# Performance work log

Hardware: AMD Instinct MI355X
Metric: run time of the kernel (lower is better)

## Reference

```python
import jax, jax.numpy as jnp
import numpy as np

B, N, H, L = 2, 512, 128, 6
NUM_T = 300.0


def setup_inputs() -> dict:
    key = jax.random.key(0)
    ks = iter(jax.random.split(key, 64))
    nrm = lambda *s: jax.random.normal(next(ks), s, dtype=jnp.float32)
    lin = lambda o, i: nrm(o, i) / np.sqrt(i)
    lin3 = lambda o, i: nrm(L, o, i) / np.sqrt(i)  # stacked per-layer weights
    return dict(
        atom_feat=nrm(B, N, 6),
        coord=nrm(B, N, 3),
        radial=jax.random.uniform(next(ks), (B, N, N, 1), dtype=jnp.float32),
        disp=nrm(B, N, N, 3),
        t=jax.random.uniform(next(ks), (B, 1), dtype=jnp.float32) * NUM_T,
        adj_mat=jnp.ones((B, N, N, 1), dtype=bool),
        mask=jnp.ones((B, N), dtype=bool),
        mask2d=jnp.ones((B, N, N, 1), dtype=bool),
        feat_enc_W=lin(H, 6), feat_enc_b=jnp.zeros(H, jnp.float32),
        freq_bands=jnp.linspace(0.0, 1.0, H // 2, dtype=jnp.float32)[None, :],
        combine_W=lin(H, 2 * H), combine_b=jnp.zeros(H, jnp.float32),
        msg_W1=lin3(H, 2 * H + 1), msg_b1=jnp.zeros((L, H), jnp.float32),
        msg_W2=lin3(H, H), msg_b2=jnp.zeros((L, H), jnp.float32),
        feat_W1=lin3(H, 2 * H), feat_b1=jnp.zeros((L, H), jnp.float32),
        feat_W2=lin3(H, H), feat_b2=jnp.zeros((L, H), jnp.float32),
        coord_W1=lin3(H, H), coord_b1=jnp.zeros((L, H), jnp.float32),
        coord_W2=lin3(1, H) * 0.001,  # xavier gain=0.001
        dec_W1=lin(H, H), dec_b1=jnp.zeros(H, jnp.float32),
        dec_W2=lin(3, H), dec_b2=jnp.zeros(3, jnp.float32),
    )


def _forward(atom_feat, coord, radial, disp, t,
             feat_enc_W, feat_enc_b, freq_bands, combine_W, combine_b,
             msg_W1, msg_b1, msg_W2, msg_b2,
             feat_W1, feat_b1, feat_W2, feat_b2,
             coord_W1, coord_b1, coord_W2,
             dec_W1, dec_b1, dec_W2, dec_b2,
             adj_mat, mask, mask2d):
    silu = jax.nn.silu
    radial = 1.0 / (radial + 0.3)  # use_rinv=True
    fenc = atom_feat @ feat_enc_W.T + feat_enc_b            # [B,N,H]
    ang = (t / NUM_T + freq_bands) * (0.5 * jnp.pi)         # [B,H/2]
    tfeat = jnp.concatenate([jnp.sin(ang), jnp.cos(ang)], -1)[:, None, :]
    tfeat = jnp.broadcast_to(tfeat, fenc.shape)
    feat = jnp.concatenate([fenc, tfeat], -1) @ combine_W.T + combine_b
    dt = feat.dtype
    maskf = mask.astype(dt)[..., None]                      # [B,N,1]
    m2f = mask2d.astype(dt)                                 # [B,N,N,1]
    adjf = adj_mat.astype(dt)
    n = feat.shape[1]
    m2nd = m2f * (1.0 - jnp.eye(n, dtype=dt))[None, :, :, None]  # diag removed
    C = jnp.sum(m2nd[:, 0, :, 0], -1, keepdims=True)[:, :, None]  # [B,1,1]

    def step(f, p):
        Wm1, bm1, Wm2, bm2, Wf1, bf1, Wf2, bf2, Wc1, bc1, Wc2 = p
        # fused broadcast-concat -> linear: split Wm1 over [feat_i | feat_j | radial]
        m = silu((f @ Wm1[:, :H].T)[:, :, None, :]
                 + (f @ Wm1[:, H:2 * H].T)[:, None, :, :]
                 + radial * Wm1[:, 2 * H] + bm1)            # [B,N,N,H]
        m = silu(m @ Wm2.T + bm2)
        # coord update (computed per EGCL, discarded by EGNN forward)
        u = silu(m @ Wc1.T + bc1) @ Wc2.T                   # [B,N,N,1]
        cu = C * jnp.sum(jnp.clip(u * disp, -100.0, 100.0) * m2f * m2nd, axis=2)
        msgf = jnp.sum(m * (m2f * adjf), axis=2)            # [B,N,H]
        nf = silu(jnp.concatenate([f, msgf], -1) @ Wf1.T + bf1) @ Wf2.T + bf2
        return nf * maskf, cu * maskf

    feat, _ = jax.lax.scan(step, feat, (msg_W1, msg_b1, msg_W2, msg_b2,
                                        feat_W1, feat_b1, feat_W2, feat_b2,
                                        coord_W1, coord_b1, coord_W2))
    new_feat = (silu(feat @ dec_W1.T + dec_b1) @ dec_W2.T + dec_b2) * maskf
    return new_feat, coord * maskf


def reference(atom_feat, coord, radial, disp, t, adj_mat, mask, mask2d,
              feat_enc_W, feat_enc_b, freq_bands, combine_W, combine_b,
              msg_W1, msg_b1, msg_W2, msg_b2,
              feat_W1, feat_b1, feat_W2, feat_b2,
              coord_W1, coord_b1, coord_W2,
              dec_W1, dec_b1, dec_W2, dec_b2):
    return _forward(atom_feat, coord, radial, disp, t,
                    feat_enc_W, feat_enc_b, freq_bands, combine_W, combine_b,
                    msg_W1, msg_b1, msg_W2, msg_b2,
                    feat_W1, feat_b1, feat_W2, feat_b2,
                    coord_W1, coord_b1, coord_W2,
                    dec_W1, dec_b1, dec_W2, dec_b2,
                    adj_mat, mask, mask2d)
```

## Files before the change

### kernel.cpp

```cpp
#include <hip/hip_runtime.h>
#include <hip/hip_bf16.h>
#include <math.h>


#define BB 2
#define NN 512
#define HH 128
#define LL 6

typedef short bf16x8 __attribute__((ext_vector_type(8)));
typedef float f32x4  __attribute__((ext_vector_type(4)));

__device__ __forceinline__ float silu_f(float x) {
    return x * __builtin_amdgcn_rcpf(1.0f + __expf(-x));
}
__device__ __forceinline__ short f2bf(float x) {
    union { __hip_bfloat16 b; short s; } u; u.b = __float2bfloat16(x); return u.s;
}
__device__ __forceinline__ float lo_bf(unsigned int w) {
    union { unsigned int u; float f; } v; v.u = w << 16; return v.f;
}
__device__ __forceinline__ float hi_bf(unsigned int w) {
    union { unsigned int u; float f; } v; v.u = w & 0xffff0000u; return v.f;
}
__device__ __forceinline__ unsigned int pk2(float a, float b) {
    return ((unsigned int)(unsigned short)f2bf(a)) |
           (((unsigned int)(unsigned short)f2bf(b)) << 16);
}

__global__ __launch_bounds__(128) void k_pack(
    const float* __restrict__ Wm2,  unsigned short* __restrict__ Wm2b,
    const float* __restrict__ Wf1,  unsigned short* __restrict__ Wf1b,
    const float* __restrict__ Wf2,  unsigned short* __restrict__ Wf2b,
    const float* __restrict__ dW1,  unsigned short* __restrict__ dW1b,
    const float* __restrict__ cmbW, unsigned short* __restrict__ cmbWb,
    const float* __restrict__ Wm1,  unsigned short* __restrict__ Wm1b,
    float* __restrict__ w3f)
{
    const int blk = blockIdx.x;
    const int h   = threadIdx.x;

    if (blk < 864) {
        const int idx4 = blk * 128 + h;
        const float* src; unsigned short* dst; int off;
        if      (idx4 < 24576)  { src = Wm2;  dst = Wm2b;  off = idx4; }
        else if (idx4 < 73728)  { src = Wf1;  dst = Wf1b;  off = idx4 - 24576; }
        else if (idx4 < 98304)  { src = Wf2;  dst = Wf2b;  off = idx4 - 73728; }
        else if (idx4 < 102400) { src = dW1;  dst = dW1b;  off = idx4 - 98304; }
        else                    { src = cmbW; dst = cmbWb; off = idx4 - 102400; }
        const float4 v = ((const float4*)src)[off];
        uint2 o; o.x = pk2(v.x, v.y); o.y = pk2(v.z, v.w);
        ((uint2*)dst)[off] = o;
        return;
    }
    const int lh = blk - 864;
    const float* srow = Wm1 + (size_t)lh * 257;
    unsigned short* drow = Wm1b + (size_t)lh * 256;
    drow[h]       = (unsigned short)f2bf(srow[h]);
    drow[h + 128] = (unsigned short)f2bf(srow[h + 128]);
    if (h == 0) w3f[lh] = srow[256];
}

__global__ __launch_bounds__(256) void k_init(
    const float* __restrict__ atom_feat, const float* __restrict__ t,
    const float* __restrict__ feat_enc_W, const float* __restrict__ feat_enc_b,
    const float* __restrict__ freq_bands,
    const unsigned short* __restrict__ cmbWb, const float* __restrict__ combine_b,
    const unsigned short* __restrict__ Wm1b,  const float* __restrict__ bm1,
    float* __restrict__ feat, float* __restrict__ Ahat,
    unsigned short* __restrict__ Bvb)
{
    const int row0 = blockIdx.x * 16;
    const int b    = row0 >> 9;
    const int tid  = threadIdx.x;
    const int w = tid >> 6, lane = tid & 63, r = lane & 15, g = lane >> 4;
    const int rswz = (r & 7) << 4;

    __shared__ float s_af[96];
    __shared__ float s_few[768];
    __shared__ float s_feb[128];
    __shared__ float s_tf[128];
    __shared__ __align__(16) unsigned short catb[16 * 256];
    __shared__ __align__(16) unsigned short fb[16 * 136];

    if (tid < 96) s_af[tid] = atom_feat[row0 * 6 + tid];
    s_few[tid]       = feat_enc_W[tid];
    s_few[tid + 256] = feat_enc_W[tid + 256];
    s_few[tid + 512] = feat_enc_W[tid + 512];
    if (tid < 128) {
        s_feb[tid] = feat_enc_b[tid];
        const float tv  = t[b] * (1.0f / 300.0f);
        const float ang = (tv + freq_bands[tid & 63]) * 1.5707963267948966f;
        s_tf[tid] = (tid < 64) ? sinf(ang) : cosf(ang);
    }
    __syncthreads();

    {
        const int rw = tid >> 4;
        const int h0 = (tid & 15) * 8;
        float f[8];
        #pragma unroll
        for (int u = 0; u < 8; ++u) {
            const int h = h0 + u;
            float acc = s_feb[h];
            #pragma unroll
            for (int k = 0; k < 6; ++k)
                acc = fmaf(s_af[rw * 6 + k], s_few[h * 6 + k], acc);
            f[u] = acc;
        }
        uint4 o;
        o.x = pk2(f[0], f[1]); o.y = pk2(f[2], f[3]);
        o.z = pk2(f[4], f[5]); o.w = pk2(f[6], f[7]);
        char* base = (char*)&catb[rw * 256];
        const int sz = (rw & 7) << 4;
        *(uint4*)(base + ((h0 * 2) ^ sz)) = o;
        uint4 o2;
        o2.x = pk2(s_tf[h0],     s_tf[h0 + 1]); o2.y = pk2(s_tf[h0 + 2], s_tf[h0 + 3]);
        o2.z = pk2(s_tf[h0 + 4], s_tf[h0 + 5]); o2.w = pk2(s_tf[h0 + 6], s_tf[h0 + 7]);
        *(uint4*)(base + ((256 + h0 * 2) ^ sz)) = o2;
    }
    __syncthreads();

    const int c0 = w * 32 + r, c1 = w * 32 + 16 + r;

    f32x4 d1a = {0,0,0,0}, d1b = {0,0,0,0};
    const char* catp = (const char*)catb;
    #pragma unroll
    for (int s = 0; s < 8; ++s) {
        bf16x8 afr = *(const bf16x8*)(catp + r * 512 + ((s*64 + g*16) ^ rswz));
        d1a = __builtin_amdgcn_mfma_f32_16x16x32_bf16(
                  afr, *(const bf16x8*)(cmbWb + (size_t)c0 * 256 + s*32 + g*8), d1a, 0,0,0);
        d1b = __builtin_amdgcn_mfma_f32_16x16x32_bf16(
                  afr, *(const bf16x8*)(cmbWb + (size_t)c1 * 256 + s*32 + g*8), d1b, 0,0,0);
    }
    {
        const float ba = combine_b[c0], bb = combine_b[c1];
        #pragma unroll
        for (int q = 0; q < 4; ++q) {
            const int rw = g * 4 + q;
            const float va = d1a[q] + ba, vb = d1b[q] + bb;
            feat[(size_t)(row0 + rw) * HH + c0] = va;
            feat[(size_t)(row0 + rw) * HH + c1] = vb;
            fb[rw * 136 + c0] = (unsigned short)f2bf(va);
            fb[rw * 136 + c1] = (unsigned short)f2bf(vb);
        }
    }
    __syncthreads();

    const char* fbp = (const char*)fb;
    f32x4 daa = {0,0,0,0}, dab = {0,0,0,0}, dba = {0,0,0,0}, dbb = {0,0,0,0};
    #pragma unroll
    for (int s = 0; s < 4; ++s) {
        bf16x8 afr = *(const bf16x8*)(fbp + r * 272 + s*64 + g*16);
        daa = __builtin_amdgcn_mfma_f32_16x16x32_bf16(
                  afr, *(const bf16x8*)(Wm1b + (size_t)c0*256 + s*32 + g*8), daa, 0,0,0);
        dab = __builtin_amdgcn_mfma_f32_16x16x32_bf16(
                  afr, *(const bf16x8*)(Wm1b + (size_t)c1*256 + s*32 + g*8), dab, 0,0,0);
        dba = __builtin_amdgcn_mfma_f32_16x16x32_bf16(
                  afr, *(const bf16x8*)(Wm1b + (size_t)c0*256 + 128 + s*32 + g*8), dba, 0,0,0);
        dbb = __builtin_amdgcn_mfma_f32_16x16x32_bf16(
                  afr, *(const bf16x8*)(Wm1b + (size_t)c1*256 + 128 + s*32 + g*8), dbb, 0,0,0);
    }
    {
        const float ba = bm1[c0], bb = bm1[c1];
        #pragma unroll
        for (int q = 0; q < 4; ++q) {
            const int rw = g * 4 + q;
            const size_t i0 = (size_t)(row0 + rw) * HH;
            Ahat[i0 + c0] = daa[q] + ba;
            Ahat[i0 + c1] = dab[q] + bb;
            Bvb[i0 + c0]  = (unsigned short)f2bf(dba[q]);
            Bvb[i0 + c1]  = (unsigned short)f2bf(dbb[q]);
        }
    }
}

__global__ __launch_bounds__(256, 2) void k_msg(
    const float* __restrict__ Ahat,
    const unsigned short* __restrict__ Bvb,
    const float* __restrict__ radial,
    const float* __restrict__ w3l,
    const unsigned short* __restrict__ Wm2b,
    const float* __restrict__ bm2,
    float* __restrict__ feat,
    const unsigned short* __restrict__ Wf1b, const float* __restrict__ bf1,
    const unsigned short* __restrict__ Wf2b, const float* __restrict__ bf2,
    const unsigned short* __restrict__ Wm1n, const float* __restrict__ bm1n,
    float* __restrict__ AhatN,
    unsigned short* __restrict__ BvbN,
    const unsigned short* __restrict__ dW1b, const float* __restrict__ db1,
    const float* __restrict__ dW2, const float* __restrict__ db2,
    const float* __restrict__ coord, float* __restrict__ out,
    int mode)
{
    const int blk  = blockIdx.x;
    const int tid  = threadIdx.x;
    const int w    = tid >> 6, lane = tid & 63, r = lane & 15, g = lane >> 4;
    const int ip   = w >> 1, jh = w & 1;
    const int i    = blk * 2 + ip;
    const int b    = i >> 9;
    const int jbase = jh * (NN / 2);

    float a_r[4][8];
    unsigned int w3p[4][4];
    #pragma unroll
    for (int s = 0; s < 4; ++s) {
        const int kb = s * 32 + g * 8;
        *(float4*)&a_r[s][0] = *(const float4*)(Ahat + (size_t)i * HH + kb);
        *(float4*)&a_r[s][4] = *(const float4*)(Ahat + (size_t)i * HH + kb + 4);
        const float4 x0 = *(const float4*)(w3l + kb);
        const float4 x1 = *(const float4*)(w3l + kb + 4);
        w3p[s][0] = pk2(x0.x, x0.y); w3p[s][1] = pk2(x0.z, x0.w);
        w3p[s][2] = pk2(x1.x, x1.y); w3p[s][3] = pk2(x1.z, x1.w);
    }

    bf16x8 bfrag[8][4];
    #pragma unroll
    for (int n = 0; n < 8; ++n)
        #pragma unroll
        for (int s = 0; s < 4; ++s)
            bfrag[n][s] = *(const bf16x8*)(Wm2b + (size_t)(n * 16 + r) * HH
                                           + s * 32 + g * 8);
    float bm2n[8];
    #pragma unroll
    for (int n = 0; n < 8; ++n) bm2n[n] = bm2[n * 16 + r];

    const unsigned short* BvB = Bvb + (size_t)b * NN * HH;
    const float* rad = radial + (size_t)i * NN;

    float msgacc[8];
    #pragma unroll
    for (int n = 0; n < 8; ++n) msgacc[n] = 0.0f;

    uint4 bv[4];
    #pragma unroll
    for (int s = 0; s < 4; ++s)
        bv[s] = *(const uint4*)(BvB + (size_t)(jbase + r) * HH + s * 32 + g * 8);
    float radv = rad[jbase + r];

    for (int c = 0; c < 16; ++c) {
        const float rinv = __builtin_amdgcn_rcpf(radv + 0.3f);

        bf16x8 afrag[4];
        #pragma unroll
        for (int s = 0; s < 4; ++s) {
            union { uint4 q; unsigned int dw[4]; } u; u.q = bv[s];
            union { bf16x8 v; unsigned int dw[4]; } o;
            #pragma unroll
            for (int d2 = 0; d2 < 4; ++d2) {
                const unsigned int bw = u.dw[d2];
                const unsigned int ww = w3p[s][d2];
                const float m0 = silu_f(fmaf(rinv, lo_bf(ww),
                                             a_r[s][d2 * 2]     + lo_bf(bw)));
                const float m1 = silu_f(fmaf(rinv, hi_bf(ww),
                                             a_r[s][d2 * 2 + 1] + hi_bf(bw)));
                o.dw[d2] = pk2(m0, m1);
            }
            afrag[s] = o.v;
        }

        if (c < 15) {
            const int j = jbase + (c + 1) * 16 + r;
            #pragma unroll
            for (int s = 0; s < 4; ++s)
                bv[s] = *(const uint4*)(BvB + (size_t)j * HH + s * 32 + g * 8);
            radv = rad[j];
        }

        #pragma unroll
        for (int n = 0; n < 8; ++n) {
            f32x4 d = {0.f, 0.f, 0.f, 0.f};
            #pragma unroll
            for (int s = 0; s < 4; ++s)
                d = __builtin_amdgcn_mfma_f32_16x16x32_bf16(
                        afrag[s], bfrag[n][s], d, 0, 0, 0);
            msgacc[n] += (silu_f(d[0] + bm2n[n]) + silu_f(d[1] + bm2n[n]))
                       + (silu_f(d[2] + bm2n[n]) + silu_f(d[3] + bm2n[n]));
        }
    }

    #pragma unroll
    for (int n = 0; n < 8; ++n) {
        float v = msgacc[n];
        v += __shfl_xor(v, 16, 64);
        v += __shfl_xor(v, 32, 64);
        msgacc[n] = v;
    }

    __shared__ float red[2][2][HH];
    __shared__ __align__(16) unsigned short catb[2 * 256];
    __shared__ __align__(16) unsigned short hidb[2 * 128];
    __shared__ __align__(16) unsigned short fb[2 * 128];
    __shared__ float hid2[2][HH];

    if (lane < 16) {
        #pragma unroll
        for (int n = 0; n < 8; ++n) red[ip][jh][n * 16 + lane] = msgacc[n];
    }
    __syncthreads();

    if (tid < 64) {
        const int rw = tid >> 5, q4 = tid & 31;
        const float4 f4 = ((const float4*)(feat + (size_t)(blk * 2 + rw) * HH))[q4];
        uint2 o; o.x = pk2(f4.x, f4.y); o.y = pk2(f4.z, f4.w);
        *(uint2*)&catb[rw * 256 + q4 * 4] = o;
    } else if (tid < 128) {
        const int rw = (tid - 64) >> 5, q4 = (tid - 64) & 31;
        const float4 m0 = ((const float4*)&red[rw][0][0])[q4];
        const float4 m1 = ((const float4*)&red[rw][1][0])[q4];
        uint2 o; o.x = pk2(m0.x + m1.x, m0.y + m1.y);
        o.y = pk2(m0.z + m1.z, m0.w + m1.w);
        *(uint2*)&catb[rw * 256 + 128 + q4 * 4] = o;
    }
    __syncthreads();

    const int c0 = w * 32 + r, c1 = w * 32 + 16 + r;
    const int rr = r & 1;

    f32x4 d1a = {0,0,0,0}, d1b = {0,0,0,0};
    #pragma unroll
    for (int s = 0; s < 8; ++s) {
        bf16x8 afr = *(const bf16x8*)((const char*)catb + rr * 512 + s*64 + g*16);
        d1a = __builtin_amdgcn_mfma_f32_16x16x32_bf16(
                  afr, *(const bf16x8*)(Wf1b + (size_t)c0 * 256 + s*32 + g*8), d1a, 0,0,0);
        d1b = __builtin_amdgcn_mfma_f32_16x16x32_bf16(
                  afr, *(const bf16x8*)(Wf1b + (size_t)c1 * 256 + s*32 + g*8), d1b, 0,0,0);
    }
    if (g == 0) {
        #pragma unroll
        for (int q = 0; q < 2; ++q) {
            hidb[q * 128 + c0] = (unsigned short)f2bf(silu_f(d1a[q] + bf1[c0]));
            hidb[q * 128 + c1] = (unsigned short)f2bf(silu_f(d1b[q] + bf1[c1]));
        }
    }
    __syncthreads();

    f32x4 d2a = {0,0,0,0}, d2b = {0,0,0,0};
    #pragma unroll
    for (int s = 0; s < 4; ++s) {
        bf16x8 afr = *(const bf16x8*)((const char*)hidb + rr * 256 + s*64 + g*16);
        d2a = __builtin_amdgcn_mfma_f32_16x16x32_bf16(
                  afr, *(const bf16x8*)(Wf2b + (size_t)c0 * 128 + s*32 + g*8), d2a, 0,0,0);
        d2b = __builtin_amdgcn_mfma_f32_16x16x32_bf16(
                  afr, *(const bf16x8*)(Wf2b + (size_t)c1 * 128 + s*32 + g*8), d2b, 0,0,0);
    }
    if (g == 0) {
        #pragma unroll
        for (int q = 0; q < 2; ++q) {
            const float va = d2a[q] + bf2[c0], vb = d2b[q] + bf2[c1];
            feat[(size_t)(blk * 2 + q) * HH + c0] = va;
            feat[(size_t)(blk * 2 + q) * HH + c1] = vb;
            fb[q * 128 + c0] = (unsigned short)f2bf(va);
            fb[q * 128 + c1] = (unsigned short)f2bf(vb);
        }
    }
    __syncthreads();

    if (mode == 0) {
        f32x4 daa = {0,0,0,0}, dab = {0,0,0,0}, dba = {0,0,0,0}, dbb = {0,0,0,0};
        #pragma unroll
        for (int s = 0; s < 4; ++s) {
            bf16x8 afr = *(const bf16x8*)((const char*)fb + rr * 256 + s*64 + g*16);
            daa = __builtin_amdgcn_mfma_f32_16x16x32_bf16(
                      afr, *(const bf16x8*)(Wm1n + (size_t)c0*256 + s*32 + g*8), daa, 0,0,0);
            dab = __builtin_amdgcn_mfma_f32_16x16x32_bf16(
                      afr, *(const bf16x8*)(Wm1n + (size_t)c1*256 + s*32 + g*8), dab, 0,0,0);
            dba = __builtin_amdgcn_mfma_f32_16x16x32_bf16(
                      afr, *(const bf16x8*)(Wm1n + (size_t)c0*256 + 128 + s*32 + g*8), dba, 0,0,0);
            dbb = __builtin_amdgcn_mfma_f32_16x16x32_bf16(
                      afr, *(const bf16x8*)(Wm1n + (size_t)c1*256 + 128 + s*32 + g*8), dbb, 0,0,0);
        }
        if (g == 0) {
            #pragma unroll
            for (int q = 0; q < 2; ++q) {
                const size_t i0 = (size_t)(blk * 2 + q) * HH;
                AhatN[i0 + c0] = daa[q] + bm1n[c0];
                AhatN[i0 + c1] = dab[q] + bm1n[c1];
                BvbN[i0 + c0]  = (unsigned short)f2bf(dba[q]);
                BvbN[i0 + c1]  = (unsigned short)f2bf(dbb[q]);
            }
        }
    } else {
        f32x4 dda = {0,0,0,0}, ddb = {0,0,0,0};
        #pragma unroll
        for (int s = 0; s < 4; ++s) {
            bf16x8 afr = *(const bf16x8*)((const char*)fb + rr * 256 + s*64 + g*16);
            dda = __builtin_amdgcn_mfma_f32_16x16x32_bf16(
                      afr, *(const bf16x8*)(dW1b + (size_t)c0 * 128 + s*32 + g*8), dda, 0,0,0);
            ddb = __builtin_amdgcn_mfma_f32_16x16x32_bf16(
                      afr, *(const bf16x8*)(dW1b + (size_t)c1 * 128 + s*32 + g*8), ddb, 0,0,0);
        }
        if (g == 0) {
            #pragma unroll
            for (int q = 0; q < 2; ++q) {
                hid2[q][c0] = silu_f(dda[q] + db1[c0]);
                hid2[q][c1] = silu_f(ddb[q] + db1[c1]);
            }
        }
        __syncthreads();
        if (tid < 6) {
            const int rw = tid / 3, c = tid - rw * 3;
            const float4* wr4 = (const float4*)(dW2 + c * HH);
            const float4* h4  = (const float4*)&hid2[rw][0];
            float a0 = db2[c], a1 = 0.f, a2 = 0.f, a3 = 0.f;
            #pragma unroll 8
            for (int k4 = 0; k4 < 32; ++k4) {
                const float4 hv = h4[k4], wv = wr4[k4];
                a0 = fmaf(hv.x, wv.x, a0); a1 = fmaf(hv.y, wv.y, a1);
                a2 = fmaf(hv.z, wv.z, a2); a3 = fmaf(hv.w, wv.w, a3);
            }
            out[(size_t)(blk * 2 + rw) * 3 + c] = (a0 + a1) + (a2 + a3);
        } else if (tid < 12) {
            const int idx = tid - 6;
            const int rw = idx / 3, c = idx - rw * 3;
            out[(size_t)BB * NN * 3 + (size_t)(blk * 2 + rw) * 3 + c] =
                coord[(size_t)(blk * 2 + rw) * 3 + c];
        }
    }
}

extern "C" void kernel_launch(void* const* d_in, const int* in_sizes, int n_in,
                              void* d_out, int out_size, void* d_ws, size_t ws_size,
                              hipStream_t stream) {
    const float* atom_feat  = (const float*)d_in[0];
    const float* coord      = (const float*)d_in[1];
    const float* radial     = (const float*)d_in[2];
    const float* t          = (const float*)d_in[4];
    const float* feat_enc_W = (const float*)d_in[8];
    const float* feat_enc_b = (const float*)d_in[9];
    const float* freq_bands = (const float*)d_in[10];
    const float* combine_W  = (const float*)d_in[11];
    const float* combine_b  = (const float*)d_in[12];
    const float* msg_W1     = (const float*)d_in[13];
    const float* msg_b1     = (const float*)d_in[14];
    const float* msg_W2     = (const float*)d_in[15];
    const float* msg_b2     = (const float*)d_in[16];
    const float* feat_W1    = (const float*)d_in[17];
    const float* feat_b1    = (const float*)d_in[18];
    const float* feat_W2    = (const float*)d_in[19];
    const float* feat_b2    = (const float*)d_in[20];
    const float* dec_W1     = (const float*)d_in[24];
    const float* dec_b1     = (const float*)d_in[25];
    const float* dec_W2     = (const float*)d_in[26];
    const float* dec_b2     = (const float*)d_in[27];

    float* feat  = (float*)d_ws;
    float* Ahat0 = feat  + (size_t)BB * NN * HH;
    float* Ahat1 = Ahat0 + (size_t)BB * NN * HH;
    float* w3f   = Ahat1 + (size_t)BB * NN * HH;
    unsigned short* Bvb0  = (unsigned short*)(w3f + LL * HH);
    unsigned short* Bvb1  = Bvb0  + (size_t)BB * NN * HH;
    unsigned short* Wm1b  = Bvb1  + (size_t)BB * NN * HH;
    unsigned short* Wm2b  = Wm1b  + (size_t)LL * HH * 256;
    unsigned short* Wf1b  = Wm2b  + (size_t)LL * HH * HH;
    unsigned short* Wf2b  = Wf1b  + (size_t)LL * HH * 256;
    unsigned short* dW1b  = Wf2b  + (size_t)LL * HH * HH;
    unsigned short* cmbWb = dW1b  + (size_t)HH * HH;

    k_pack<<<1632, 128, 0, stream>>>(
        msg_W2, Wm2b, feat_W1, Wf1b, feat_W2, Wf2b,
        dec_W1, dW1b, combine_W, cmbWb, msg_W1, Wm1b, w3f);

    k_init<<<BB * NN / 16, 256, 0, stream>>>(
        atom_feat, t, feat_enc_W, feat_enc_b, freq_bands,
        cmbWb, combine_b, Wm1b, msg_b1, feat, Ahat0, Bvb0);

    float*          AhatP[2] = {Ahat0, Ahat1};
    unsigned short* BvbP[2]  = {Bvb0, Bvb1};

    for (int l = 0; l < LL; ++l) {
        const int cur = l & 1, nxt = cur ^ 1;
        const int last = (l == LL - 1);
        k_msg<<<BB * NN / 2, 256, 0, stream>>>(
            AhatP[cur], BvbP[cur], radial, w3f + l * HH,
            Wm2b + (size_t)l * HH * HH, msg_b2 + l * HH,
            feat,
            Wf1b + (size_t)l * HH * 256, feat_b1 + l * HH,
            Wf2b + (size_t)l * HH * HH,  feat_b2 + l * HH,
            Wm1b + (size_t)(last ? 0 : (l + 1)) * HH * 256,
            msg_b1 + (last ? 0 : (l + 1)) * HH,
            AhatP[nxt], BvbP[nxt],
            dW1b, dec_b1, dec_W2, dec_b2,
            coord, (float*)d_out,
            last ? 1 : 0);
    }
}
```

Before: 469.5 us.

## Split message kernel over K halves with LDS exchange, one row per block

Each block now handles a single node i instead of two, and its four waves split into two j-halves times two K-halves of the hidden dimension. Each wave computes only half of the edge-message activations and swaps them through a double-buffered, swizzled LDS buffer, so every wave holds half the Wm2 output columns and half the register fragments. The aim is to cut register pressure (launch bounds raised to 3 blocks per CU) and double the grid for better occupancy. In exchange it adds a __syncthreads per j-chunk and LDS traffic, and the per-node feature MLP tail now leaves three of the four MFMA rows unused.

```diff
diff --git a/kernel.cpp b/kernel.cpp
--- a/kernel.cpp
+++ b/kernel.cpp
@@ -175,7 +175,7 @@
     }
 }
 
-__global__ __launch_bounds__(256, 2) void k_msg(
+__global__ __launch_bounds__(256, 3) void k_msg(
     const float* __restrict__ Ahat,
     const unsigned short* __restrict__ Bvb,
     const float* __restrict__ radial,
@@ -193,19 +193,20 @@
     const float* __restrict__ coord, float* __restrict__ out,
     int mode)
 {
-    const int blk  = blockIdx.x;
+    const int i    = blockIdx.x;
+    const int b    = i >> 9;
     const int tid  = threadIdx.x;
     const int w    = tid >> 6, lane = tid & 63, r = lane & 15, g = lane >> 4;
-    const int ip   = w >> 1, jh = w & 1;
-    const int i    = blk * 2 + ip;
-    const int b    = i >> 9;
-    const int jbase = jh * (NN / 2);
-
-    float a_r[4][8];
-    unsigned int w3p[4][4];
-    #pragma unroll
-    for (int s = 0; s < 4; ++s) {
-        const int kb = s * 32 + g * 8;
+    const int jq   = w >> 1, kh = w & 1;
+    const int jbase = jq * (NN / 2);
+    const int k0   = kh * 64;
+    const int swz  = (r & 7) << 4;
+
+    float a_r[2][8];
+    unsigned int w3p[2][4];
+    #pragma unroll
+    for (int s = 0; s < 2; ++s) {
+        const int kb = k0 + s * 32 + g * 8;
         *(float4*)&a_r[s][0] = *(const float4*)(Ahat + (size_t)i * HH + kb);
         *(float4*)&a_r[s][4] = *(const float4*)(Ahat + (size_t)i * HH + kb + 4);
         const float4 x0 = *(const float4*)(w3l + kb);
@@ -214,145 +215,145 @@
         w3p[s][2] = pk2(x1.x, x1.y); w3p[s][3] = pk2(x1.z, x1.w);
     }
 
-    bf16x8 bfrag[8][4];
-    #pragma unroll
-    for (int n = 0; n < 8; ++n)
-        #pragma unroll
-        for (int s = 0; s < 4; ++s)
-            bfrag[n][s] = *(const bf16x8*)(Wm2b + (size_t)(n * 16 + r) * HH
-                                           + s * 32 + g * 8);
-    float bm2n[8];
-    #pragma unroll
-    for (int n = 0; n < 8; ++n) bm2n[n] = bm2[n * 16 + r];
+    bf16x8 bfragO[4][4];
+    #pragma unroll
+    for (int nl = 0; nl < 4; ++nl) {
+        const size_t row = (size_t)((kh * 4 + nl) * 16 + r) * HH;
+        bfragO[nl][0] = *(const bf16x8*)(Wm2b + row + k0 + g * 8);
+        bfragO[nl][1] = *(const bf16x8*)(Wm2b + row + k0 + 32 + g * 8);
+        bfragO[nl][2] = *(const bf16x8*)(Wm2b + row + (k0 ^ 64) + g * 8);
+        bfragO[nl][3] = *(const bf16x8*)(Wm2b + row + (k0 ^ 64) + 32 + g * 8);
+    }
+    float bm2n[4];
+    #pragma unroll
+    for (int nl = 0; nl < 4; ++nl) bm2n[nl] = bm2[(kh * 4 + nl) * 16 + r];
 
     const unsigned short* BvB = Bvb + (size_t)b * NN * HH;
     const float* rad = radial + (size_t)i * NN;
 
-    float msgacc[8];
-    #pragma unroll
-    for (int n = 0; n < 8; ++n) msgacc[n] = 0.0f;
-
-    uint4 bv[4];
-    #pragma unroll
-    for (int s = 0; s < 4; ++s)
-        bv[s] = *(const uint4*)(BvB + (size_t)(jbase + r) * HH + s * 32 + g * 8);
+    __shared__ __align__(16) unsigned short af_lds[2][2][2][1024];
+
+    float msgacc[4] = {0.f, 0.f, 0.f, 0.f};
+
+    uint4 bv0 = *(const uint4*)(BvB + (size_t)(jbase + r) * HH + k0 + g * 8);
+    uint4 bv1 = *(const uint4*)(BvB + (size_t)(jbase + r) * HH + k0 + 32 + g * 8);
     float radv = rad[jbase + r];
 
+    int p = 0;
     for (int c = 0; c < 16; ++c) {
         const float rinv = __builtin_amdgcn_rcpf(radv + 0.3f);
 
-        bf16x8 afrag[4];
-        #pragma unroll
-        for (int s = 0; s < 4; ++s) {
-            union { uint4 q; unsigned int dw[4]; } u; u.q = bv[s];
-            union { bf16x8 v; unsigned int dw[4]; } o;
+        union { bf16x8 v; uint4 q; unsigned int dw[4]; } o0, o1;
+        {
+            union { uint4 q; unsigned int dw[4]; } u0, u1;
+            u0.q = bv0; u1.q = bv1;
             #pragma unroll
             for (int d2 = 0; d2 < 4; ++d2) {
-                const unsigned int bw = u.dw[d2];
-                const unsigned int ww = w3p[s][d2];
-                const float m0 = silu_f(fmaf(rinv, lo_bf(ww),
-                                             a_r[s][d2 * 2]     + lo_bf(bw)));
-                const float m1 = silu_f(fmaf(rinv, hi_bf(ww),
-                                             a_r[s][d2 * 2 + 1] + hi_bf(bw)));
-                o.dw[d2] = pk2(m0, m1);
+                const unsigned int bw = u0.dw[d2], ww = w3p[0][d2];
+                const float m0 = silu_f(fmaf(rinv, lo_bf(ww), a_r[0][d2*2]   + lo_bf(bw)));
+                const float m1 = silu_f(fmaf(rinv, hi_bf(ww), a_r[0][d2*2+1] + hi_bf(bw)));
+                o0.dw[d2] = pk2(m0, m1);
             }
-            afrag[s] = o.v;
+            #pragma unroll
+            for (int d2 = 0; d2 < 4; ++d2) {
+                const unsigned int bw = u1.dw[d2], ww = w3p[1][d2];
+                const float m0 = silu_f(fmaf(rinv, lo_bf(ww), a_r[1][d2*2]   + lo_bf(bw)));
+                const float m1 = silu_f(fmaf(rinv, hi_bf(ww), a_r[1][d2*2+1] + hi_bf(bw)));
+                o1.dw[d2] = pk2(m0, m1);
+            }
+        }
+
+        {
+            char* wb = (char*)&af_lds[p][jq][kh][0] + r * 128;
+            *(uint4*)(wb + ((g * 16) ^ swz))      = o0.q;
+            *(uint4*)(wb + ((64 + g * 16) ^ swz)) = o1.q;
         }
 
         if (c < 15) {
             const int j = jbase + (c + 1) * 16 + r;
-            #pragma unroll
-            for (int s = 0; s < 4; ++s)
-                bv[s] = *(const uint4*)(BvB + (size_t)j * HH + s * 32 + g * 8);
+            bv0 = *(const uint4*)(BvB + (size_t)j * HH + k0 + g * 8);
+            bv1 = *(const uint4*)(BvB + (size_t)j * HH + k0 + 32 + g * 8);
             radv = rad[j];
         }
 
-        #pragma unroll
-        for (int n = 0; n < 8; ++n) {
+        __syncthreads();
+
+        const char* rb = (const char*)&af_lds[p][jq][kh ^ 1][0] + r * 128;
+        const bf16x8 part0 = *(const bf16x8*)(rb + ((g * 16) ^ swz));
+        const bf16x8 part1 = *(const bf16x8*)(rb + ((64 + g * 16) ^ swz));
+
+        #pragma unroll
+        for (int nl = 0; nl < 4; ++nl) {
             f32x4 d = {0.f, 0.f, 0.f, 0.f};
-            #pragma unroll
-            for (int s = 0; s < 4; ++s)
-                d = __builtin_amdgcn_mfma_f32_16x16x32_bf16(
-                        afrag[s], bfrag[n][s], d, 0, 0, 0);
-            msgacc[n] += (silu_f(d[0] + bm2n[n]) + silu_f(d[1] + bm2n[n]))
-                       + (silu_f(d[2] + bm2n[n]) + silu_f(d[3] + bm2n[n]));
-        }
-    }
-
-    #pragma unroll
-    for (int n = 0; n < 8; ++n) {
-        float v = msgacc[n];
+            d = __builtin_amdgcn_mfma_f32_16x16x32_bf16(o0.v,  bfragO[nl][0], d, 0, 0, 0);
+            d = __builtin_amdgcn_mfma_f32_16x16x32_bf16(o1.v,  bfragO[nl][1], d, 0, 0, 0);
+            d = __builtin_amdgcn_mfma_f32_16x16x32_bf16(part0, bfragO[nl][2], d, 0, 0, 0);
+            d = __builtin_amdgcn_mfma_f32_16x16x32_bf16(part1, bfragO[nl][3], d, 0, 0, 0);
+            msgacc[nl] += (silu_f(d[0] + bm2n[nl]) + silu_f(d[1] + bm2n[nl]))
+                        + (silu_f(d[2] + bm2n[nl]) + silu_f(d[3] + bm2n[nl]));
+        }
+        p ^= 1;
+    }
+
+    #pragma unroll
+    for (int nl = 0; nl < 4; ++nl) {
+        float v = msgacc[nl];
         v += __shfl_xor(v, 16, 64);
         v += __shfl_xor(v, 32, 64);
-        msgacc[n] = v;
-    }
-
-    __shared__ float red[2][2][HH];
-    __shared__ __align__(16) unsigned short catb[2 * 256];
-    __shared__ __align__(16) unsigned short hidb[2 * 128];
-    __shared__ __align__(16) unsigned short fb[2 * 128];
-    __shared__ float hid2[2][HH];
+        msgacc[nl] = v;
+    }
+
+    __shared__ float red[2][HH];
+    __shared__ __align__(16) unsigned short catb[256];
+    __shared__ __align__(16) unsigned short hidb[HH];
+    __shared__ __align__(16) unsigned short fbb[HH];
+    __shared__ float hid2[HH];
 
     if (lane < 16) {
         #pragma unroll
-        for (int n = 0; n < 8; ++n) red[ip][jh][n * 16 + lane] = msgacc[n];
-    }
-    __syncthreads();
-
-    if (tid < 64) {
-        const int rw = tid >> 5, q4 = tid & 31;
-        const float4 f4 = ((const float4*)(feat + (size_t)(blk * 2 + rw) * HH))[q4];
-        uint2 o; o.x = pk2(f4.x, f4.y); o.y = pk2(f4.z, f4.w);
-        *(uint2*)&catb[rw * 256 + q4 * 4] = o;
-    } else if (tid < 128) {
-        const int rw = (tid - 64) >> 5, q4 = (tid - 64) & 31;
-        const float4 m0 = ((const float4*)&red[rw][0][0])[q4];
-        const float4 m1 = ((const float4*)&red[rw][1][0])[q4];
-        uint2 o; o.x = pk2(m0.x + m1.x, m0.y + m1.y);
-        o.y = pk2(m0.z + m1.z, m0.w + m1.w);
-        *(uint2*)&catb[rw * 256 + 128 + q4 * 4] = o;
-    }
-    __syncthreads();
-
-    const int c0 = w * 32 + r, c1 = w * 32 + 16 + r;
-    const int rr = r & 1;
+        for (int nl = 0; nl < 4; ++nl)
+            red[jq][(kh * 4 + nl) * 16 + lane] = msgacc[nl];
+    }
+    __syncthreads();
+
+    if (tid < 128) {
+        catb[tid]       = (unsigned short)f2bf(feat[(size_t)i * HH + tid]);
+        catb[128 + tid] = (unsigned short)f2bf(red[0][tid] + red[1][tid]);
+    }
+    __syncthreads();
+
+    const int c0 = w * 32 + r, c1 = c0 + 16;
 
     f32x4 d1a = {0,0,0,0}, d1b = {0,0,0,0};
     #pragma unroll
     for (int s = 0; s < 8; ++s) {
-        bf16x8 afr = *(const bf16x8*)((const char*)catb + rr * 512 + s*64 + g*16);
+        bf16x8 afr = *(const bf16x8*)((const char*)catb + s * 64 + g * 16);
         d1a = __builtin_amdgcn_mfma_f32_16x16x32_bf16(
                   afr, *(const bf16x8*)(Wf1b + (size_t)c0 * 256 + s*32 + g*8), d1a, 0,0,0);
         d1b = __builtin_amdgcn_mfma_f32_16x16x32_bf16(
                   afr, *(const bf16x8*)(Wf1b + (size_t)c1 * 256 + s*32 + g*8), d1b, 0,0,0);
     }
     if (g == 0) {
-        #pragma unroll
-        for (int q = 0; q < 2; ++q) {
-            hidb[q * 128 + c0] = (unsigned short)f2bf(silu_f(d1a[q] + bf1[c0]));
-            hidb[q * 128 + c1] = (unsigned short)f2bf(silu_f(d1b[q] + bf1[c1]));
-        }
+        hidb[c0] = (unsigned short)f2bf(silu_f(d1a[0] + bf1[c0]));
+        hidb[c1] = (unsigned short)f2bf(silu_f(d1b[0] + bf1[c1]));
     }
     __syncthreads();
 
     f32x4 d2a = {0,0,0,0}, d2b = {0,0,0,0};
     #pragma unroll
     for (int s = 0; s < 4; ++s) {
-        bf16x8 afr = *(const bf16x8*)((const char*)hidb + rr * 256 + s*64 + g*16);
+        bf16x8 afr = *(const bf16x8*)((const char*)hidb + s * 64 + g * 16);
         d2a = __builtin_amdgcn_mfma_f32_16x16x32_bf16(
                   afr, *(const bf16x8*)(Wf2b + (size_t)c0 * 128 + s*32 + g*8), d2a, 0,0,0);
         d2b = __builtin_amdgcn_mfma_f32_16x16x32_bf16(
                   afr, *(const bf16x8*)(Wf2b + (size_t)c1 * 128 + s*32 + g*8), d2b, 0,0,0);
     }
     if (g == 0) {
-        #pragma unroll
-        for (int q = 0; q < 2; ++q) {
-            const float va = d2a[q] + bf2[c0], vb = d2b[q] + bf2[c1];
-            feat[(size_t)(blk * 2 + q) * HH + c0] = va;
-            feat[(size_t)(blk * 2 + q) * HH + c1] = vb;
-            fb[q * 128 + c0] = (unsigned short)f2bf(va);
-            fb[q * 128 + c1] = (unsigned short)f2bf(vb);
-        }
+        const float va = d2a[0] + bf2[c0], vb = d2b[0] + bf2[c1];
+        feat[(size_t)i * HH + c0] = va;
+        feat[(size_t)i * HH + c1] = vb;
+        fbb[c0] = (unsigned short)f2bf(va);
+        fbb[c1] = (unsigned short)f2bf(vb);
     }
     __syncthreads();
 
@@ -360,7 +361,7 @@
         f32x4 daa = {0,0,0,0}, dab = {0,0,0,0}, dba = {0,0,0,0}, dbb = {0,0,0,0};
         #pragma unroll
         for (int s = 0; s < 4; ++s) {
-            bf16x8 afr = *(const bf16x8*)((const char*)fb + rr * 256 + s*64 + g*16);
+            bf16x8 afr = *(const bf16x8*)((const char*)fbb + s * 64 + g * 16);
             daa = __builtin_amdgcn_mfma_f32_16x16x32_bf16(
                       afr, *(const bf16x8*)(Wm1n + (size_t)c0*256 + s*32 + g*8), daa, 0,0,0);
             dab = __builtin_amdgcn_mfma_f32_16x16x32_bf16(
@@ -371,50 +372,41 @@
                       afr, *(const bf16x8*)(Wm1n + (size_t)c1*256 + 128 + s*32 + g*8), dbb, 0,0,0);
         }
         if (g == 0) {
-            #pragma unroll
-            for (int q = 0; q < 2; ++q) {
-                const size_t i0 = (size_t)(blk * 2 + q) * HH;
-                AhatN[i0 + c0] = daa[q] + bm1n[c0];
-                AhatN[i0 + c1] = dab[q] + bm1n[c1];
-                BvbN[i0 + c0]  = (unsigned short)f2bf(dba[q]);
-                BvbN[i0 + c1]  = (unsigned short)f2bf(dbb[q]);
-            }
+            const size_t i0 = (size_t)i * HH;
+            AhatN[i0 + c0] = daa[0] + bm1n[c0];
+            AhatN[i0 + c1] = dab[0] + bm1n[c1];
+            BvbN[i0 + c0]  = (unsigned short)f2bf(dba[0]);
+            BvbN[i0 + c1]  = (unsigned short)f2bf(dbb[0]);
         }
     } else {
         f32x4 dda = {0,0,0,0}, ddb = {0,0,0,0};
         #pragma unroll
         for (int s = 0; s < 4; ++s) {
-            bf16x8 afr = *(const bf16x8*)((const char*)fb + rr * 256 + s*64 + g*16);
+            bf16x8 afr = *(const bf16x8*)((const char*)fbb + s * 64 + g * 16);
             dda = __builtin_amdgcn_mfma_f32_16x16x32_bf16(
                       afr, *(const bf16x8*)(dW1b + (size_t)c0 * 128 + s*32 + g*8), dda, 0,0,0);
             ddb = __builtin_amdgcn_mfma_f32_16x16x32_bf16(
                       afr, *(const bf16x8*)(dW1b + (size_t)c1 * 128 + s*32 + g*8), ddb, 0,0,0);
         }
         if (g == 0) {
-            #pragma unroll
-            for (int q = 0; q < 2; ++q) {
-                hid2[q][c0] = silu_f(dda[q] + db1[c0]);
-                hid2[q][c1] = silu_f(ddb[q] + db1[c1]);
-            }
+            hid2[c0] = silu_f(dda[0] + db1[c0]);
+            hid2[c1] = silu_f(ddb[0] + db1[c1]);
         }
         __syncthreads();
-        if (tid < 6) {
-            const int rw = tid / 3, c = tid - rw * 3;
-            const float4* wr4 = (const float4*)(dW2 + c * HH);
-            const float4* h4  = (const float4*)&hid2[rw][0];
-            float a0 = db2[c], a1 = 0.f, a2 = 0.f, a3 = 0.f;
+        if (tid < 3) {
+            const float4* wr4 = (const float4*)(dW2 + tid * HH);
+            const float4* h4  = (const float4*)hid2;
+            float a0 = db2[tid], a1 = 0.f, a2 = 0.f, a3 = 0.f;
             #pragma unroll 8
             for (int k4 = 0; k4 < 32; ++k4) {
                 const float4 hv = h4[k4], wv = wr4[k4];
                 a0 = fmaf(hv.x, wv.x, a0); a1 = fmaf(hv.y, wv.y, a1);
                 a2 = fmaf(hv.z, wv.z, a2); a3 = fmaf(hv.w, wv.w, a3);
             }
-            out[(size_t)(blk * 2 + rw) * 3 + c] = (a0 + a1) + (a2 + a3);
-        } else if (tid < 12) {
-            const int idx = tid - 6;
-            const int rw = idx / 3, c = idx - rw * 3;
-            out[(size_t)BB * NN * 3 + (size_t)(blk * 2 + rw) * 3 + c] =
-                coord[(size_t)(blk * 2 + rw) * 3 + c];
+            out[(size_t)i * 3 + tid] = (a0 + a1) + (a2 + a3);
+        } else if (tid >= 4 && tid < 7) {
+            const int c = tid - 4;
+            out[(size_t)BB * NN * 3 + (size_t)i * 3 + c] = coord[(size_t)i * 3 + c];
         }
     }
 }
@@ -471,7 +463,7 @@
     for (int l = 0; l < LL; ++l) {
         const int cur = l & 1, nxt = cur ^ 1;
         const int last = (l == LL - 1);
-        k_msg<<<BB * NN / 2, 256, 0, stream>>>(
+        k_msg<<<BB * NN, 256, 0, stream>>>(
             AhatP[cur], BvbP[cur], radial, w3f + l * HH,
             Wm2b + (size_t)l * HH * HH, msg_b2 + l * HH,
             feat,
```

After: 457.0 us. -2.7%, faster.
